# Kernel tuning notes

Hardware: AMD Instinct MI355X
Metric: run time of the kernel (lower is better)

Reference implementation:

```python
import jax, jax.numpy as jnp
import numpy as np

B, N, DIM, H = 32, 480, 1024, 16


def setup_inputs() -> dict:
    key = jax.random.key(0)
    ks = jax.random.split(key, 7)
    s = 0.02
    return {
        "q": jax.random.normal(ks[0], (B, N, DIM), jnp.float32),
        "Wq": jax.random.normal(ks[1], (DIM, DIM), jnp.float32) * s,
        "Wk": jax.random.normal(ks[2], (DIM, DIM), jnp.float32) * s,
        "Wv": jax.random.normal(ks[3], (DIM, DIM), jnp.float32) * s,
        "pe": jax.random.normal(ks[4], (480, 480), jnp.float32),
        "Wo": jax.random.normal(ks[5], (DIM, DIM), jnp.float32) * s,
        "bo": jnp.zeros((DIM,), jnp.float32),
    }


def reference(q, Wq, Wk, Wv, pe, Wo, bo):
    b, n, dim = q.shape
    h = H
    d = dim // h
    scale = d ** -0.5
    # self-attention: k = v = q (pre-projection)
    qp = (q @ Wq.T).reshape(b, n, h, d).transpose(0, 2, 1, 3)  # b h n d
    kp = (q @ Wk.T).reshape(b, n, h, d).transpose(0, 2, 1, 3)
    vp = (q @ Wv.T).reshape(b, n, h, d).transpose(0, 2, 1, 3)
    dots = jnp.einsum("bhid,bhjd->bhij", qp, kp) * scale
    dots = dots + pe[:n, :n]  # learned additive positional bias
    attn = jax.nn.softmax(dots, axis=-1)
    out = jnp.einsum("bhij,bhjd->bhid", attn, vp)
    out = out.transpose(0, 2, 1, 3).reshape(b, n, dim)
    return out @ Wo.T + bo
```

## Files before the change

### kernel.cpp

```cpp
#include <hip/hip_runtime.h>
#include <hip/hip_bf16.h>
#include <stdint.h>

#define B_   32
#define N_   480
#define DIM_ 1024
#define H_   16
#define D_   64
#define M_   (B_*N_)
#define BH_  (B_*H_)

typedef __bf16 bf16;
typedef __bf16 bf16x4 __attribute__((ext_vector_type(4)));
typedef __bf16 bf16x8 __attribute__((ext_vector_type(8)));
typedef short  short4v __attribute__((ext_vector_type(4)));
typedef float  f32x4  __attribute__((ext_vector_type(4)));

__device__ __forceinline__ void gld_lds16(const void* g, void* l) {
    using GP = const __attribute__((address_space(1))) unsigned int*;
    using LP = __attribute__((address_space(3))) unsigned int*;
    __builtin_amdgcn_global_load_lds((GP)(uintptr_t)g, (LP)(unsigned int)(uintptr_t)l, 16, 0, 0);
}

__global__ void cvt4(const float* __restrict__ in, bf16* __restrict__ out, int n4) {
    int i = blockIdx.x * 256 + threadIdx.x;
    if (i >= n4) return;
    float4 v = ((const float4*)in)[i];
    bf16x4 o = { (bf16)v.x, (bf16)v.y, (bf16)v.z, (bf16)v.w };
    ((bf16x4*)out)[i] = o;
}

__global__ void cvtW(const float* __restrict__ Wq, const float* __restrict__ Wk,
                     const float* __restrict__ Wv, const float* __restrict__ Wo,
                     bf16* __restrict__ Wcat, bf16* __restrict__ Wob) {
    int i = blockIdx.x * 256 + threadIdx.x;
    const float* src; bf16* dst;
    switch (blockIdx.y) {
        case 0: src = Wq; dst = Wcat;                break;
        case 1: src = Wk; dst = Wcat + DIM_*DIM_;    break;
        case 2: src = Wv; dst = Wcat + 2*DIM_*DIM_;  break;
        default: src = Wo; dst = Wob;                break;
    }
    float4 v = ((const float4*)src)[i];
    bf16x4 o = { (bf16)v.x, (bf16)v.y, (bf16)v.z, (bf16)v.w };
    ((bf16x4*)dst)[i] = o;
}

#define GEMM_PRE()                                                            \
    const int tid  = threadIdx.x;                                             \
    const int lane = tid & 63;                                                \
    const int wid  = tid >> 6;                                                \
    const int wm   = wid & 1, wn = wid >> 1;                                  \
    const int m0   = blockIdx.y * 128;                                        \
    const int n0   = blockIdx.x * 128;                                        \
    const int lm   = lane & 15, lq = lane >> 4;                               \
    const int aLane = (lane >> 3) * 1024 + (((lane & 7) ^ (lane >> 3)) & 7) * 8; \
    const bf16* Asrc = A  + (m0 + wid*32) * 1024 + aLane;                     \
    const bf16* Bsrc = Bw + (n0 + wid*32) * 1024 + aLane;                     \
    bf16* AsDst = As + (wid*32)*64;                                           \
    bf16* BsDst = Bs + (wid*32)*64;                                           \
    int rowA[4], rowB[4];                                                     \
    _Pragma("unroll") for (int m = 0; m < 4; ++m) rowA[m] = (wm*64 + m*16 + lm)*64; \
    _Pragma("unroll") for (int n = 0; n < 4; ++n) rowB[n] = (wn*64 + n*16 + lm)*64; \
    const int sw = lm & 7;                                                    \
    int phys[2];                                                              \
    phys[0] = ((lq)     ^ sw) * 8;                                            \
    phys[1] = ((4 + lq) ^ sw) * 8;

#define GEMM_KLOOP(FIRST, SECOND)                                             \
    for (int k0 = 0; k0 < 1024; k0 += 64) {                                   \
        _Pragma("unroll") for (int j = 0; j < 4; ++j) {                       \
            gld_lds16(Asrc + k0 + j*8192, AsDst + j*512);                     \
            gld_lds16(Bsrc + k0 + j*8192, BsDst + j*512);                     \
        }                                                                     \
        __syncthreads();                                                      \
        _Pragma("unroll") for (int ks = 0; ks < 2; ++ks) {                    \
            bf16x8 af[4], bfr[4];                                             \
            _Pragma("unroll") for (int m = 0; m < 4; ++m)                     \
                af[m]  = *(const bf16x8*)&As[rowA[m] + phys[ks]];             \
            _Pragma("unroll") for (int n = 0; n < 4; ++n)                     \
                bfr[n] = *(const bf16x8*)&Bs[rowB[n] + phys[ks]];             \
            _Pragma("unroll") for (int m = 0; m < 4; ++m)                     \
                _Pragma("unroll") for (int n = 0; n < 4; ++n)                 \
                    acc[m][n] = __builtin_amdgcn_mfma_f32_16x16x32_bf16(      \
                        FIRST, SECOND, acc[m][n], 0, 0, 0);                   \
        }                                                                     \
        __syncthreads();                                                      \
    }

__global__ __launch_bounds__(256) void gemm_qkv(const bf16* __restrict__ A, const bf16* __restrict__ Bw,
                                                bf16* __restrict__ Qp, bf16* __restrict__ Kp,
                                                bf16* __restrict__ Vt) {
    __shared__ bf16 As[128*64];
    __shared__ bf16 Bs[128*64];
    GEMM_PRE();
    const int part = n0 >> 10;
    f32x4 acc[4][4] = {};

    if (part != 2) {
        GEMM_KLOOP(af[m], bfr[n]);
        bf16* dst = (part == 0) ? Qp : Kp;
        int hh[4], dd[4];
#pragma unroll
        for (int n = 0; n < 4; ++n) {
            int rem = (n0 + wn*64 + n*16 + lm) & 1023;
            hh[n] = rem >> 6; dd[n] = rem & 63;
        }
#pragma unroll
        for (int m = 0; m < 4; ++m) {
#pragma unroll
            for (int r = 0; r < 4; ++r) {
                int gm = m0 + wm*64 + m*16 + lq*4 + r;
                int b  = gm / 480;
                int nn = gm - b*480;
#pragma unroll
                for (int n = 0; n < 4; ++n)
                    dst[((b*16 + hh[n])*480 + nn)*64 + dd[n]] = (bf16)acc[m][n][r];
            }
        }
    } else {
        GEMM_KLOOP(bfr[n], af[m]);
#pragma unroll
        for (int m = 0; m < 4; ++m) {
            int gmBase = m0 + wm*64 + m*16;
            int b  = gmBase / 480;
            int nn = gmBase - b*480 + lm;
#pragma unroll
            for (int n = 0; n < 4; ++n)
#pragma unroll
                for (int r = 0; r < 4; ++r) {
                    int rem = (n0 + wn*64 + n*16 + lq*4 + r) & 1023;
                    int h = rem >> 6, d = rem & 63;
                    Vt[((b*16 + h)*64 + d)*480 + nn] = (bf16)acc[m][n][r];
                }
        }
    }
}

#define KT 96
#define OS_LD 72
__global__ __launch_bounds__(320, 4) void attn(const bf16* __restrict__ Qp, const bf16* __restrict__ Kp,
                                               const bf16* __restrict__ Vt, const float* __restrict__ pe,
                                               bf16* __restrict__ O) {
    __shared__ bf16 Ks[KT*64];
    __shared__ bf16 Vs[64*128];
    char* KsB = (char*)Ks;
    char* VsB = (char*)Vs;
    const int tid  = threadIdx.x;
    const int lane = tid & 63, wid = tid >> 6;
    const int bh   = blockIdx.y;
    const int b    = bh >> 4, h = bh & 15;
    const int qblk = blockIdx.x * 80;
    const int lm   = lane & 15, lq = lane >> 4;
    const int qbase = bh * (N_ * 64);

    const bool has2 = tid < 128;
    int kLds[3];
#pragma unroll
    for (int i = 0; i < 3; ++i) {
        int id = tid + i*320, r = id >> 3, c = id & 7;
        kLds[i] = r*128 + ((c ^ (r & 7)) << 4);
    }
    int vLds[3], vGE[3];
#pragma unroll
    for (int i = 0; i < 3; ++i) {
        int id = tid + i*320, r = id / 12, c = id - r*12;
        vLds[i] = r*256 + (((c & 8) | ((c & 7) ^ (r & 7))) << 4);
        vGE[i]  = (bh*64 + r)*480 + c*8;
    }

    bf16x8 qb[2];
#pragma unroll
    for (int ks = 0; ks < 2; ++ks)
        qb[ks] = *(const bf16x8*)&Qp[qbase + (qblk + wid*16 + lm)*64 + ks*32 + lq*8];
    const float* peP = pe + (qblk + wid*16 + lm)*480 + lq*4;

    int kOff[2];
#pragma unroll
    for (int ks = 0; ks < 2; ++ks) kOff[ks] = ((ks*4 + lq) ^ (lm & 7)) << 4;
    int vOff[6];
#pragma unroll
    for (int mf = 0; mf < 6; ++mf) {
        int c = 2*mf + (lq >> 1);
        vOff[mf] = (((c & 8) | ((c & 7) ^ (lm & 7))) << 4) + (lq & 1)*8;
    }

    uint4 kreg[3], vreg[3];
#define LOAD_TILE(T)                                                          \
    {   const char* kg = (const char*)Kp + (size_t)(qbase + (T)*KT*64)*2;     \
        kreg[0] = *(const uint4*)(kg + tid*16);                               \
        kreg[1] = *(const uint4*)(kg + tid*16 + 5120);                        \
        if (has2) kreg[2] = *(const uint4*)(kg + tid*16 + 10240);             \
        vreg[0] = *(const uint4*)((const char*)Vt + (size_t)(vGE[0] + (T)*KT)*2); \
        vreg[1] = *(const uint4*)((const char*)Vt + (size_t)(vGE[1] + (T)*KT)*2); \
        if (has2) vreg[2] = *(const uint4*)((const char*)Vt + (size_t)(vGE[2] + (T)*KT)*2); }

    LOAD_TILE(0);

    f32x4 ot[4] = {};
    float lsum = 0.f;

    for (int kt = 0; kt < 5; ++kt) {
        if (kt) __syncthreads();
        *(uint4*)(KsB + kLds[0]) = kreg[0];
        *(uint4*)(KsB + kLds[1]) = kreg[1];
        if (has2) *(uint4*)(KsB + kLds[2]) = kreg[2];
        *(uint4*)(VsB + vLds[0]) = vreg[0];
        *(uint4*)(VsB + vLds[1]) = vreg[1];
        if (has2) *(uint4*)(VsB + vLds[2]) = vreg[2];
        __syncthreads();
        if (kt < 4) LOAD_TILE(kt + 1);

        short4v pb[6];
#pragma unroll
        for (int mf = 0; mf < 6; ++mf) {
            f32x4 s = {};
#pragma unroll
            for (int ks = 0; ks < 2; ++ks) {
                bf16x8 ka = *(const bf16x8*)(KsB + (mf*16 + lm)*128 + kOff[ks]);
                s = __builtin_amdgcn_mfma_f32_16x16x32_bf16(ka, qb[ks], s, 0, 0, 0);
            }
            f32x4 pe4 = *(const f32x4*)(peP + kt*KT + mf*16);
            bf16x4 pv;
#pragma unroll
            for (int r = 0; r < 4; ++r) {
                float e = __expf(s[r] * 0.125f + pe4[r]);
                lsum += e;
                pv[r] = (bf16)e;
            }
            pb[mf] = __builtin_bit_cast(short4v, pv);
        }

#pragma unroll
        for (int df = 0; df < 4; ++df) {
            const char* vrow = VsB + (df*16 + lm)*256;
#pragma unroll
            for (int mf = 0; mf < 6; ++mf) {
                short4v va = *(const short4v*)(vrow + vOff[mf]);
                ot[df] = __builtin_amdgcn_mfma_f32_16x16x16bf16_1k(va, pb[mf], ot[df], 0, 0, 0);
            }
        }
    }
#undef LOAD_TILE

    lsum += __shfl_xor(lsum, 16);
    lsum += __shfl_xor(lsum, 32);
    float rl = 1.f / lsum;

    __syncthreads();
    bf16* Os = Ks;
#pragma unroll
    for (int df = 0; df < 4; ++df)
#pragma unroll
        for (int r = 0; r < 4; ++r)
            Os[(wid*16 + lm)*OS_LD + df*16 + lq*4 + r] = (bf16)(ot[df][r] * rl);
    __syncthreads();
    for (int c = tid; c < 640; c += 320) {
        int row = c >> 3, d0 = (c & 7) * 8;
        uint4 u = *(const uint4*)&Os[row*OS_LD + d0];
        *(uint4*)&O[(b*480 + qblk + row)*1024 + h*64 + d0] = u;
    }
}

__global__ __launch_bounds__(256) void gemm_out(const bf16* __restrict__ A, const bf16* __restrict__ Bw,
                                                const float* __restrict__ bo, float* __restrict__ out) {
    __shared__ bf16 As[128*64];
    __shared__ bf16 Bs[128*64];
    GEMM_PRE();
    f32x4 acc[4][4] = {};
    GEMM_KLOOP(af[m], bfr[n]);
#pragma unroll
    for (int m = 0; m < 4; ++m)
#pragma unroll
        for (int n = 0; n < 4; ++n)
#pragma unroll
            for (int r = 0; r < 4; ++r) {
                int gm = m0 + wm*64 + m*16 + lq*4 + r;
                int gn = n0 + wn*64 + n*16 + lm;
                out[gm*1024 + gn] = acc[m][n][r] + bo[gn];
            }
}

extern "C" void kernel_launch(void* const* d_in, const int* in_sizes, int n_in,
                              void* d_out, int out_size, void* d_ws, size_t ws_size,
                              hipStream_t stream) {
    const float* q  = (const float*)d_in[0];
    const float* Wq = (const float*)d_in[1];
    const float* Wk = (const float*)d_in[2];
    const float* Wv = (const float*)d_in[3];
    const float* pe = (const float*)d_in[4];
    const float* Wo = (const float*)d_in[5];
    const float* bo = (const float*)d_in[6];
    float* out = (float*)d_out;

    char* ws = (char*)d_ws;
    bf16* Abf  = (bf16*)(ws);
    bf16* Wcat = (bf16*)(ws + 31457280);
    bf16* Wob  = (bf16*)(ws + 31457280 + 6291456);
    bf16* Qp   = (bf16*)(ws + 39845888);
    bf16* Kp   = (bf16*)(ws + 71303168);
    bf16* Vt   = (bf16*)(ws + 102760448);

    cvt4<<<(M_*DIM_/4 + 255)/256, 256, 0, stream>>>(q, Abf, M_*DIM_/4);
    cvtW<<<dim3(DIM_*DIM_/4/256, 4), 256, 0, stream>>>(Wq, Wk, Wv, Wo, Wcat, Wob);

    gemm_qkv<<<dim3(24, 120), 256, 0, stream>>>(Abf, Wcat, Qp, Kp, Vt);
    attn<<<dim3(6, 512), 320, 0, stream>>>(Qp, Kp, Vt, pe, Abf);
    gemm_out<<<dim3(8, 120), 256, 0, stream>>>(Abf, Wob, bo, out);
}
```

Before: 477.6 us.

## Double-buffer attention K/V tiles via direct global-to-LDS loads

The attention kernel now double-buffers its K and V tiles in shared memory and fills them with asynchronous global_load_lds writes, replacing the register-staged copy. This removes the register round trip and one barrier per tile. Blocks grow from 5 to 6 waves, covering 96 query rows each, so the grid shrinks from 6 to 5 blocks per head. The positional-bias values are now prefetched at the start of each tile. In exchange, LDS use doubles and occupancy drops to 3 blocks per CU. The V swizzle relies on clamping the column index to stay in bounds.

Result: faster. 417.8 us (-12.5%).

```diff
diff --git a/kernel.cpp b/kernel.cpp
--- a/kernel.cpp
+++ b/kernel.cpp
@@ -139,34 +139,29 @@
 
 #define KT 96
 #define OS_LD 72
-__global__ __launch_bounds__(320, 4) void attn(const bf16* __restrict__ Qp, const bf16* __restrict__ Kp,
+__global__ __launch_bounds__(384, 3) void attn(const bf16* __restrict__ Qp, const bf16* __restrict__ Kp,
                                                const bf16* __restrict__ Vt, const float* __restrict__ pe,
                                                bf16* __restrict__ O) {
-    __shared__ bf16 Ks[KT*64];
-    __shared__ bf16 Vs[64*128];
-    char* KsB = (char*)Ks;
-    char* VsB = (char*)Vs;
+    __shared__ bf16 Ks[2][KT*64];
+    __shared__ bf16 Vs[2][64*128];
     const int tid  = threadIdx.x;
     const int lane = tid & 63, wid = tid >> 6;
     const int bh   = blockIdx.y;
     const int b    = bh >> 4, h = bh & 15;
-    const int qblk = blockIdx.x * 80;
+    const int qblk = blockIdx.x * 96;
     const int lm   = lane & 15, lq = lane >> 4;
     const int qbase = bh * (N_ * 64);
 
-    const bool has2 = tid < 128;
-    int kLds[3];
+    const int kROff = (lane >> 3)*64 + ((lane & 7) ^ (lane >> 3))*8;
+    int vOffG[3];
 #pragma unroll
     for (int i = 0; i < 3; ++i) {
-        int id = tid + i*320, r = id >> 3, c = id & 7;
-        kLds[i] = r*128 + ((c ^ (r & 7)) << 4);
-    }
-    int vLds[3], vGE[3];
-#pragma unroll
-    for (int i = 0; i < 3; ++i) {
-        int id = tid + i*320, r = id / 12, c = id - r*12;
-        vLds[i] = r*256 + (((c & 8) | ((c & 7) ^ (r & 7))) << 4);
-        vGE[i]  = (bh*64 + r)*480 + c*8;
+        int j = wid + 6*i;
+        int r = j*4 + (lane >> 4);
+        int p = lane & 15;
+        int c = (p & 8) | ((p & 7) ^ (r & 7));
+        if (c > 11) c = 11;
+        vOffG[i] = (bh*64 + r)*480 + c*8;
     }
 
     bf16x8 qb[2];
@@ -185,31 +180,32 @@
         vOff[mf] = (((c & 8) | ((c & 7) ^ (lm & 7))) << 4) + (lq & 1)*8;
     }
 
-    uint4 kreg[3], vreg[3];
-#define LOAD_TILE(T)                                                          \
-    {   const char* kg = (const char*)Kp + (size_t)(qbase + (T)*KT*64)*2;     \
-        kreg[0] = *(const uint4*)(kg + tid*16);                               \
-        kreg[1] = *(const uint4*)(kg + tid*16 + 5120);                        \
-        if (has2) kreg[2] = *(const uint4*)(kg + tid*16 + 10240);             \
-        vreg[0] = *(const uint4*)((const char*)Vt + (size_t)(vGE[0] + (T)*KT)*2); \
-        vreg[1] = *(const uint4*)((const char*)Vt + (size_t)(vGE[1] + (T)*KT)*2); \
-        if (has2) vreg[2] = *(const uint4*)((const char*)Vt + (size_t)(vGE[2] + (T)*KT)*2); }
-
-    LOAD_TILE(0);
+#define STAGE(T, BUF)                                                         \
+    {   const bf16* kg = Kp + qbase + (T)*(KT*64);                            \
+        char* kd = (char*)Ks[BUF];                                            \
+        gld_lds16(kg + (wid*2 + 0)*512 + kROff, kd + (wid*2 + 0)*1024);       \
+        gld_lds16(kg + (wid*2 + 1)*512 + kROff, kd + (wid*2 + 1)*1024);       \
+        char* vd = (char*)Vs[BUF];                                            \
+        _Pragma("unroll") for (int i = 0; i < 3; ++i) {                       \
+            int j = wid + 6*i;                                                \
+            if (j < 16) gld_lds16(Vt + vOffG[i] + (T)*KT, vd + j*1024);       \
+        } }
+
+    STAGE(0, 0);
 
     f32x4 ot[4] = {};
     float lsum = 0.f;
 
     for (int kt = 0; kt < 5; ++kt) {
-        if (kt) __syncthreads();
-        *(uint4*)(KsB + kLds[0]) = kreg[0];
-        *(uint4*)(KsB + kLds[1]) = kreg[1];
-        if (has2) *(uint4*)(KsB + kLds[2]) = kreg[2];
-        *(uint4*)(VsB + vLds[0]) = vreg[0];
-        *(uint4*)(VsB + vLds[1]) = vreg[1];
-        if (has2) *(uint4*)(VsB + vLds[2]) = vreg[2];
+        const int cur = kt & 1;
         __syncthreads();
-        if (kt < 4) LOAD_TILE(kt + 1);
+        f32x4 pe4[6];
+#pragma unroll
+        for (int mf = 0; mf < 6; ++mf)
+            pe4[mf] = *(const f32x4*)(peP + kt*KT + mf*16);
+        if (kt < 4) STAGE(kt + 1, cur ^ 1);
+        const char* KsB = (const char*)Ks[cur];
+        const char* VsB = (const char*)Vs[cur];
 
         short4v pb[6];
 #pragma unroll
@@ -220,11 +216,10 @@
                 bf16x8 ka = *(const bf16x8*)(KsB + (mf*16 + lm)*128 + kOff[ks]);
                 s = __builtin_amdgcn_mfma_f32_16x16x32_bf16(ka, qb[ks], s, 0, 0, 0);
             }
-            f32x4 pe4 = *(const f32x4*)(peP + kt*KT + mf*16);
             bf16x4 pv;
 #pragma unroll
             for (int r = 0; r < 4; ++r) {
-                float e = __expf(s[r] * 0.125f + pe4[r]);
+                float e = __expf(s[r] * 0.125f + pe4[mf][r]);
                 lsum += e;
                 pv[r] = (bf16)e;
             }
@@ -241,21 +236,21 @@
             }
         }
     }
-#undef LOAD_TILE
+#undef STAGE
 
     lsum += __shfl_xor(lsum, 16);
     lsum += __shfl_xor(lsum, 32);
     float rl = 1.f / lsum;
 
     __syncthreads();
-    bf16* Os = Ks;
+    bf16* Os = &Ks[0][0];
 #pragma unroll
     for (int df = 0; df < 4; ++df)
 #pragma unroll
         for (int r = 0; r < 4; ++r)
             Os[(wid*16 + lm)*OS_LD + df*16 + lq*4 + r] = (bf16)(ot[df][r] * rl);
     __syncthreads();
-    for (int c = tid; c < 640; c += 320) {
+    for (int c = tid; c < 768; c += 384) {
         int row = c >> 3, d0 = (c & 7) * 8;
         uint4 u = *(const uint4*)&Os[row*OS_LD + d0];
         *(uint4*)&O[(b*480 + qblk + row)*1024 + h*64 + d0] = u;
@@ -305,6 +300,6 @@
     cvtW<<<dim3(DIM_*DIM_/4/256, 4), 256, 0, stream>>>(Wq, Wk, Wv, Wo, Wcat, Wob);
 
     gemm_qkv<<<dim3(24, 120), 256, 0, stream>>>(Abf, Wcat, Qp, Kp, Vt);
-    attn<<<dim3(6, 512), 320, 0, stream>>>(Qp, Kp, Vt, pe, Abf);
+    attn<<<dim3(5, 512), 384, 0, stream>>>(Qp, Kp, Vt, pe, Abf);
     gemm_out<<<dim3(8, 120), 256, 0, stream>>>(Abf, Wob, bo, out);
 }
```
